# Performance work log

Hardware: AMD Instinct MI355X
Metric: run time of the kernel (lower is better)

## Reference

```python
import jax, jax.numpy as jnp
import numpy as np

B, D, H = 16384, 2048, 16
EPS = 1e-5


def setup_inputs() -> dict:
    key = jax.random.key(0)
    ks = jax.random.split(key, 14)
    s = 0.02
    return {
        "e_a": jax.random.normal(ks[0], (B, D), jnp.float32),
        "e_b": jax.random.normal(ks[1], (B, D), jnp.float32),
        "w_in_ab": jax.random.normal(ks[2], (3 * D, D), jnp.float32) * s,
        "b_in_ab": jnp.zeros((3 * D,), jnp.float32),
        "w_out_ab": jax.random.normal(ks[3], (D, D), jnp.float32) * s,
        "b_out_ab": jnp.zeros((D,), jnp.float32),
        "w_in_ba": jax.random.normal(ks[4], (3 * D, D), jnp.float32) * s,
        "b_in_ba": jnp.zeros((3 * D,), jnp.float32),
        "w_out_ba": jax.random.normal(ks[5], (D, D), jnp.float32) * s,
        "b_out_ba": jnp.zeros((D,), jnp.float32),
        "gamma_a": jnp.ones((D,), jnp.float32),
        "beta_a": jnp.zeros((D,), jnp.float32),
        "gamma_b": jnp.ones((D,), jnp.float32),
        "beta_b": jnp.zeros((D,), jnp.float32),
    }


def _mha_seq1(q_in, kv_in, w_in, b_in, w_out, b_out):
    """torch nn.MultiheadAttention with seq_len=1 for both query and key."""
    b, d = q_in.shape
    hd = d // H
    wq, wk, wv = jnp.split(w_in, 3, axis=0)
    bq, bk, bv = jnp.split(b_in, 3)
    q = (q_in @ wq.T + bq).reshape(b, H, hd)
    k = (kv_in @ wk.T + bk).reshape(b, H, hd)
    v = (kv_in @ wv.T + bv).reshape(b, H, hd)
    scores = jnp.sum(q * k, axis=-1) / jnp.sqrt(jnp.asarray(hd, q.dtype))  # (B,H)
    w = jax.nn.softmax(scores[..., None], axis=-1)  # (B,H,1) == ones (single key)
    attn = (w * v).reshape(b, d)
    out = attn @ w_out.T + b_out
    attn_w = jnp.mean(w, axis=1)[:, None, :]  # (B,1,1), averaged over heads
    return out, attn_w


def _layernorm(x, g, b):
    m = jnp.mean(x, axis=-1, keepdims=True)
    v = jnp.mean((x - m) ** 2, axis=-1, keepdims=True)
    return (x - m) / jnp.sqrt(v + EPS) * g + b


def reference(e_a, e_b, w_in_ab, b_in_ab, w_out_ab, b_out_ab,
              w_in_ba, b_in_ba, w_out_ba, b_out_ba,
              gamma_a, beta_a, gamma_b, beta_b):
    a_attn, attn_w_a = _mha_seq1(e_a, e_b, w_in_ab, b_in_ab, w_out_ab, b_out_ab)
    b_attn, _ = _mha_seq1(e_b, e_a, w_in_ba, b_in_ba, w_out_ba, b_out_ba)
    e_a_prime = _layernorm(e_a + a_attn, gamma_a, beta_a)
    e_b_prime = _layernorm(e_b + b_attn, gamma_b, beta_b)
    return (e_a_prime, e_b_prime, attn_w_a)
```

## Files before the change

### kernel.cpp

```cpp
#include <hip/hip_runtime.h>
#include <hip/hip_bf16.h>
#include <stdint.h>
#include <stddef.h>


static constexpr int B_ROWS = 16384;
static constexpr int DIM    = 2048;
static constexpr float EPS  = 1e-5f;

typedef __bf16 bf16_t;
typedef __bf16 bf16x8 __attribute__((ext_vector_type(8)));
typedef float  f32x4  __attribute__((ext_vector_type(4)));

#define MEMFENCE asm volatile("" ::: "memory")
#define SBAR     __builtin_amdgcn_s_barrier()
#define SCHEDB   __builtin_amdgcn_sched_barrier(0)
#define WAITVM(n) asm volatile("s_waitcnt vmcnt(" #n ")" ::: "memory")

__device__ __forceinline__ void gld_lds16(const bf16_t* g, bf16_t* l) {
  __builtin_amdgcn_global_load_lds(
      (const __attribute__((address_space(1))) void*)g,
      (__attribute__((address_space(3))) void*)l, 16, 0, 0);
}

__global__ __launch_bounds__(256) void k_f32_to_bf16(const float* __restrict__ in,
                                                     bf16_t* __restrict__ out) {
  size_t i = ((size_t)blockIdx.x * 256 + threadIdx.x) * 8;
  f32x4 a = *(const f32x4*)(in + i);
  f32x4 b = *(const f32x4*)(in + i + 4);
  bf16x8 o;
  o[0] = (bf16_t)a[0]; o[1] = (bf16_t)a[1]; o[2] = (bf16_t)a[2]; o[3] = (bf16_t)a[3];
  o[4] = (bf16_t)b[0]; o[5] = (bf16_t)b[1]; o[6] = (bf16_t)b[2]; o[7] = (bf16_t)b[3];
  *(bf16x8*)(out + i) = o;
}

__global__ __launch_bounds__(256) void k_transpose_bf16(const float* __restrict__ W,
                                                        bf16_t* __restrict__ Wt,
                                                        int n) {
  __shared__ float t[32][33];
  const int bx = blockIdx.x * 32, by = blockIdx.y * 32;
  const int tx = threadIdx.x & 31, ty = threadIdx.x >> 5;
  #pragma unroll
  for (int r = ty; r < 32; r += 8)
    t[r][tx] = W[(size_t)(by + r) * n + bx + tx];
  __syncthreads();
  #pragma unroll
  for (int r = ty; r < 32; r += 8)
    Wt[(size_t)(bx + r) * n + by + tx] = (bf16_t)t[tx][r];
}

__global__ __launch_bounds__(256) void k_bias_combine(const float* __restrict__ wout,
                                                      const float* __restrict__ bv,
                                                      const float* __restrict__ bout,
                                                      float* __restrict__ bc, int n) {
  const int i = blockIdx.x;
  const float* row = wout + (size_t)i * n;
  float s = 0.f;
  for (int k = threadIdx.x; k < n; k += 256) s += row[k] * bv[k];
  #pragma unroll
  for (int o = 32; o; o >>= 1) s += __shfl_down(s, o, 64);
  __shared__ float red[4];
  if ((threadIdx.x & 63) == 0) red[threadIdx.x >> 6] = s;
  __syncthreads();
  if (threadIdx.x == 0) bc[i] = red[0] + red[1] + red[2] + red[3] + bout[i];
}

__global__ __launch_bounds__(256) void k_gemm_bt_small(const bf16_t* __restrict__ A,
                                                       const bf16_t* __restrict__ Bt,
                                                       bf16_t* __restrict__ Cb,
                                                       int M, int N, int K) {
  __shared__ bf16_t lA[128 * 32];
  __shared__ bf16_t lB[128 * 32];
  const int tid  = threadIdx.x;
  const int lane = tid & 63;
  const int wid  = tid >> 6;
  const int wm = wid >> 1, wn = wid & 1;
  const int m0 = blockIdx.y * 128, n0 = blockIdx.x * 128;

  const int sr = tid >> 2;
  const int sc = (tid & 3) * 8;
  const bf16_t* gA0 = A  + (size_t)(m0 + sr) * K + sc;
  const bf16_t* gA1 = A  + (size_t)(m0 + 64 + sr) * K + sc;
  const bf16_t* gB0 = Bt + (size_t)(n0 + sr) * K + sc;
  const bf16_t* gB1 = Bt + (size_t)(n0 + 64 + sr) * K + sc;

  f32x4 acc[4][4] = {};
  const int fr = lane & 15;
  const int kh = (lane >> 4) * 8;

  for (int kt = 0; kt < K; kt += 32) {
    gld_lds16(gA0 + kt, lA + tid * 8);
    gld_lds16(gA1 + kt, lA + 2048 + tid * 8);
    gld_lds16(gB0 + kt, lB + tid * 8);
    gld_lds16(gB1 + kt, lB + 2048 + tid * 8);
    __syncthreads();
    bf16x8 af[4], bfv[4];
    #pragma unroll
    for (int i = 0; i < 4; ++i) {
      af[i]  = *(const bf16x8*)(lA + (wm * 64 + i * 16 + fr) * 32 + kh);
      bfv[i] = *(const bf16x8*)(lB + (wn * 64 + i * 16 + fr) * 32 + kh);
    }
    #pragma unroll
    for (int i = 0; i < 4; ++i)
      #pragma unroll
      for (int j = 0; j < 4; ++j)
        acc[i][j] = __builtin_amdgcn_mfma_f32_16x16x32_bf16(af[i], bfv[j], acc[i][j], 0, 0, 0);
    __syncthreads();
  }
  const int cr = (lane >> 4) * 4;
  const int cc = lane & 15;
  #pragma unroll
  for (int i = 0; i < 4; ++i)
    #pragma unroll
    for (int j = 0; j < 4; ++j) {
      const int gm = m0 + wm * 64 + i * 16 + cr;
      const int gn = n0 + wn * 64 + j * 16 + cc;
      #pragma unroll
      for (int r = 0; r < 4; ++r)
        Cb[(size_t)(gm + r) * N + gn] = (bf16_t)acc[i][j][r];
    }
}

__global__ __launch_bounds__(512, 2) void k_gemm256(const bf16_t* __restrict__ A,
                                                    const bf16_t* __restrict__ Bt,
                                                    float* __restrict__ Cf,
                                                    const float* __restrict__ resid,
                                                    const float* __restrict__ bias,
                                                    int M, int N, int K) {
  __shared__ bf16_t lA[2][256 * 64];
  __shared__ bf16_t lB[2][256 * 64];
  const int tid  = threadIdx.x;
  const int lane = tid & 63;
  const int wid  = tid >> 6;
  const int wr = wid >> 2;
  const int wc = wid & 3;

  const int nbx = N >> 8;
  const int nwg = (M >> 8) * nbx;
  const int orig = blockIdx.y * nbx + blockIdx.x;
  const int cpx = nwg >> 3;
  const int swz = (orig & 7) * cpx + (orig >> 3);
  const int m0 = (swz / nbx) << 8;
  const int n0 = (swz % nbx) << 8;

  const int srow  = tid >> 3;
  const int sunit = (tid & 7) ^ ((tid >> 3) & 7);
  const bf16_t* gA = A  + (size_t)(m0 + srow) * K + sunit * 8;
  const bf16_t* gB = Bt + (size_t)(n0 + srow) * K + sunit * 8;
  const size_t cK = (size_t)64 * K;
  const int lofs = tid * 8;

  f32x4 acc[8][4] = {};

  const int NT = K >> 6;

  const int frl = lane & 15;
  const int fxor = lane & 7;
  const int fg  = lane >> 4;

#define LDA(buf, i, kk) \
  (*(const bf16x8*)(&lA[buf][(wr * 128 + (i) * 16 + frl) * 64 + \
                            ((((kk) * 4 + fg) ^ fxor) * 8)]))
#define LDB(buf, j, kk) \
  (*(const bf16x8*)(&lB[buf][(wc * 64 + (j) * 16 + frl) * 64 + \
                            ((((kk) * 4 + fg) ^ fxor) * 8)]))
#define STAGE_A(buf, c, kt) gld_lds16(gA + (size_t)(c) * cK + (kt), \
                                      &lA[buf][(c) * 4096 + lofs])
#define STAGE_B(buf, c, kt) gld_lds16(gB + (size_t)(c) * cK + (kt), \
                                      &lB[buf][(c) * 4096 + lofs])

#define MFMA16(mg, kk)                                                         \
  __builtin_amdgcn_s_setprio(1);                                               \
  _Pragma("unroll")                                                            \
  for (int mi = 0; mi < 4; ++mi) {                                             \
    _Pragma("unroll")                                                          \
    for (int j = 0; j < 4; ++j)                                                \
      acc[(mg) * 4 + mi][j] = __builtin_amdgcn_mfma_f32_16x16x32_bf16(         \
          af[mi], bf[j], acc[(mg) * 4 + mi][j], 0, 0, 0);                      \
  }                                                                            \
  __builtin_amdgcn_s_setprio(0)

  {
    STAGE_B(0, 0, 0); STAGE_B(0, 1, 0); STAGE_B(0, 2, 0); STAGE_B(0, 3, 0);
    STAGE_A(0, 0, 0); STAGE_A(0, 2, 0); STAGE_A(0, 1, 0); STAGE_A(0, 3, 0);
    WAITVM(0); SCHEDB;
    MEMFENCE; SBAR; MEMFENCE;
  }

  bf16x8 bf[4];
  int buf = 0;

  for (int t = 0; t < NT - 1; ++t) {
    const int ktn = (t + 1) << 6;
    const int nb = buf ^ 1;
    {
      bf16x8 af[4];
      #pragma unroll
      for (int mi = 0; mi < 4; ++mi) af[mi] = LDA(buf, mi, 0);
      #pragma unroll
      for (int j = 0; j < 4; ++j) bf[j] = LDB(buf, j, 0);
      STAGE_B(nb, 0, ktn); STAGE_B(nb, 1, ktn);
      MEMFENCE; SBAR; MEMFENCE;
      MFMA16(0, 0);
      WAITVM(2); SCHEDB;
      MEMFENCE; SBAR; MEMFENCE;
    }
    {
      bf16x8 af[4];
      #pragma unroll
      for (int mi = 0; mi < 4; ++mi) af[mi] = LDA(buf, 4 + mi, 0);
      STAGE_B(nb, 2, ktn); STAGE_B(nb, 3, ktn);
      MEMFENCE; SBAR; MEMFENCE;
      MFMA16(1, 0);
      MEMFENCE; SBAR; MEMFENCE;
    }
    {
      bf16x8 af[4];
      #pragma unroll
      for (int mi = 0; mi < 4; ++mi) af[mi] = LDA(buf, mi, 1);
      #pragma unroll
      for (int j = 0; j < 4; ++j) bf[j] = LDB(buf, j, 1);
      STAGE_A(nb, 0, ktn); STAGE_A(nb, 2, ktn);
      MEMFENCE; SBAR; MEMFENCE;
      MFMA16(0, 1);
      MEMFENCE; SBAR; MEMFENCE;
    }
    {
      bf16x8 af[4];
      #pragma unroll
      for (int mi = 0; mi < 4; ++mi) af[mi] = LDA(buf, 4 + mi, 1);
      STAGE_A(nb, 1, ktn); STAGE_A(nb, 3, ktn);
      MEMFENCE; SBAR; MEMFENCE;
      MFMA16(1, 1);
      WAITVM(2); SCHEDB;
      MEMFENCE; SBAR; MEMFENCE;
    }
    buf = nb;
  }

  {
    {
      bf16x8 af[4];
      #pragma unroll
      for (int mi = 0; mi < 4; ++mi) af[mi] = LDA(buf, mi, 0);
      #pragma unroll
      for (int j = 0; j < 4; ++j) bf[j] = LDB(buf, j, 0);
      MEMFENCE; SBAR; MEMFENCE;
      MFMA16(0, 0);
      WAITVM(0); SCHEDB;
      MEMFENCE; SBAR; MEMFENCE;
    }
    {
      bf16x8 af[4];
      #pragma unroll
      for (int mi = 0; mi < 4; ++mi) af[mi] = LDA(buf, 4 + mi, 0);
      MEMFENCE; SBAR; MEMFENCE;
      MFMA16(1, 0);
      MEMFENCE; SBAR; MEMFENCE;
    }
    {
      bf16x8 af[4];
      #pragma unroll
      for (int mi = 0; mi < 4; ++mi) af[mi] = LDA(buf, mi, 1);
      #pragma unroll
      for (int j = 0; j < 4; ++j) bf[j] = LDB(buf, j, 1);
      MEMFENCE; SBAR; MEMFENCE;
      MFMA16(0, 1);
      MEMFENCE; SBAR; MEMFENCE;
    }
    {
      bf16x8 af[4];
      #pragma unroll
      for (int mi = 0; mi < 4; ++mi) af[mi] = LDA(buf, 4 + mi, 1);
      MEMFENCE; SBAR; MEMFENCE;
      MFMA16(1, 1);
    }
  }

  const int cr = (lane >> 4) * 4;
  const int cc = lane & 15;
  #pragma unroll
  for (int i = 0; i < 8; ++i) {
    #pragma unroll
    for (int j = 0; j < 4; ++j) {
      const int gm = m0 + wr * 128 + i * 16 + cr;
      const int gn = n0 + wc * 64 + j * 16 + cc;
      #pragma unroll
      for (int r = 0; r < 4; ++r) {
        const size_t idx = (size_t)(gm + r) * N + gn;
        Cf[idx] = acc[i][j][r] + resid[idx] + bias[gn];
      }
    }
  }
#undef LDA
#undef LDB
#undef STAGE_A
#undef STAGE_B
#undef MFMA16
}

__global__ __launch_bounds__(256) void k_ln(float* __restrict__ io,
                                            const float* __restrict__ gamma_a,
                                            const float* __restrict__ beta_a,
                                            const float* __restrict__ gamma_b,
                                            const float* __restrict__ beta_b) {
  const int row = blockIdx.x;
  const float* gamma = (row < B_ROWS) ? gamma_a : gamma_b;
  const float* beta  = (row < B_ROWS) ? beta_a  : beta_b;
  float* p = io + (size_t)row * DIM;
  const int c0 = threadIdx.x * 8;

  f32x4 x0 = *(f32x4*)(p + c0);
  f32x4 x1 = *(f32x4*)(p + c0 + 4);
  float s = 0.f, sq = 0.f;
  #pragma unroll
  for (int r = 0; r < 4; ++r) {
    s += x0[r] + x1[r];
    sq += x0[r] * x0[r] + x1[r] * x1[r];
  }
  #pragma unroll
  for (int o = 32; o; o >>= 1) {
    s  += __shfl_down(s, o, 64);
    sq += __shfl_down(sq, o, 64);
  }
  __shared__ float rs[4], rq[4];
  if ((threadIdx.x & 63) == 0) { rs[threadIdx.x >> 6] = s; rq[threadIdx.x >> 6] = sq; }
  __syncthreads();
  s  = rs[0] + rs[1] + rs[2] + rs[3];
  sq = rq[0] + rq[1] + rq[2] + rq[3];

  const float mean = s * (1.f / DIM);
  const float var  = sq * (1.f / DIM) - mean * mean;
  const float inv  = rsqrtf(var + EPS);

  f32x4 g0 = *(const f32x4*)(gamma + c0);
  f32x4 g1 = *(const f32x4*)(gamma + c0 + 4);
  f32x4 b0 = *(const f32x4*)(beta + c0);
  f32x4 b1 = *(const f32x4*)(beta + c0 + 4);
  #pragma unroll
  for (int r = 0; r < 4; ++r) {
    x0[r] = (x0[r] - mean) * inv * g0[r] + b0[r];
    x1[r] = (x1[r] - mean) * inv * g1[r] + b1[r];
  }
  *(f32x4*)(p + c0)     = x0;
  *(f32x4*)(p + c0 + 4) = x1;
}

__global__ __launch_bounds__(256) void k_fill_ones(float* __restrict__ p, int n) {
  const int i = blockIdx.x * 256 + threadIdx.x;
  if (i < n) p[i] = 1.0f;
}

extern "C" void kernel_launch(void* const* d_in, const int* in_sizes, int n_in,
                              void* d_out, int out_size, void* d_ws, size_t ws_size,
                              hipStream_t stream) {
  const float* e_a      = (const float*)d_in[0];
  const float* e_b      = (const float*)d_in[1];
  const float* w_in_ab  = (const float*)d_in[2];
  const float* b_in_ab  = (const float*)d_in[3];
  const float* w_out_ab = (const float*)d_in[4];
  const float* b_out_ab = (const float*)d_in[5];
  const float* w_in_ba  = (const float*)d_in[6];
  const float* b_in_ba  = (const float*)d_in[7];
  const float* w_out_ba = (const float*)d_in[8];
  const float* b_out_ba = (const float*)d_in[9];
  const float* gamma_a  = (const float*)d_in[10];
  const float* beta_a   = (const float*)d_in[11];
  const float* gamma_b  = (const float*)d_in[12];
  const float* beta_b   = (const float*)d_in[13];
  float* out = (float*)d_out;

  char* w = (char*)d_ws;
  bf16_t* eA_bf  = (bf16_t*)w; w += (size_t)B_ROWS * DIM * 2;
  bf16_t* eB_bf  = (bf16_t*)w; w += (size_t)B_ROWS * DIM * 2;
  bf16_t* woAB   = (bf16_t*)w; w += (size_t)DIM * DIM * 2;
  bf16_t* woBA   = (bf16_t*)w; w += (size_t)DIM * DIM * 2;
  bf16_t* wvTAB  = (bf16_t*)w; w += (size_t)DIM * DIM * 2;
  bf16_t* wvTBA  = (bf16_t*)w; w += (size_t)DIM * DIM * 2;
  bf16_t* wcAB   = (bf16_t*)w; w += (size_t)DIM * DIM * 2;
  bf16_t* wcBA   = (bf16_t*)w; w += (size_t)DIM * DIM * 2;
  float*  bcAB   = (float*)w;  w += (size_t)DIM * 4;
  float*  bcBA   = (float*)w;  w += (size_t)DIM * 4;

  const size_t nE = (size_t)B_ROWS * DIM;
  const size_t nW = (size_t)DIM * DIM;

  k_f32_to_bf16<<<nE / 2048, 256, 0, stream>>>(e_a, eA_bf);
  k_f32_to_bf16<<<nE / 2048, 256, 0, stream>>>(e_b, eB_bf);
  k_f32_to_bf16<<<nW / 2048, 256, 0, stream>>>(w_out_ab, woAB);
  k_f32_to_bf16<<<nW / 2048, 256, 0, stream>>>(w_out_ba, woBA);
  k_transpose_bf16<<<dim3(64, 64), 256, 0, stream>>>(w_in_ab + 2 * nW, wvTAB, DIM);
  k_transpose_bf16<<<dim3(64, 64), 256, 0, stream>>>(w_in_ba + 2 * nW, wvTBA, DIM);
  k_bias_combine<<<DIM, 256, 0, stream>>>(w_out_ab, b_in_ab + 2 * DIM, b_out_ab, bcAB, DIM);
  k_bias_combine<<<DIM, 256, 0, stream>>>(w_out_ba, b_in_ba + 2 * DIM, b_out_ba, bcBA, DIM);

  k_gemm_bt_small<<<dim3(16, 16), 256, 0, stream>>>(woAB, wvTAB, wcAB, DIM, DIM, DIM);
  k_gemm_bt_small<<<dim3(16, 16), 256, 0, stream>>>(woBA, wvTBA, wcBA, DIM, DIM, DIM);

  k_gemm256<<<dim3(8, 64), 512, 0, stream>>>(eB_bf, wcAB, out,      e_a, bcAB,
                                             B_ROWS, DIM, DIM);
  k_gemm256<<<dim3(8, 64), 512, 0, stream>>>(eA_bf, wcBA, out + nE, e_b, bcBA,
                                             B_ROWS, DIM, DIM);

  k_ln<<<2 * B_ROWS, 256, 0, stream>>>(out, gamma_a, beta_a, gamma_b, beta_b);

  k_fill_ones<<<(B_ROWS + 255) / 256, 256, 0, stream>>>(out + 2 * nE, B_ROWS);
}
```

Measured before the change: 1.071 ms.

## Split-K weight-combine GEMM, merge conversions, reorder staging, grid-stride layernorm

The small weight-combine GEMMs now use an 8-way split-K grid that accumulates with fp32 atomics into a zeroed scratch buffer (aliased over the start of the workspace), followed by a conversion to bf16. The activation and weight f32-to-bf16 conversions are merged into paired launches, and activation conversion happens after the scratch is consumed. The main GEMM's prefetch order is changed to stage A before B, and layernorm becomes a grid-stride loop with fewer blocks. The aim is better occupancy for the small GEMM and fewer launches. The cost is atomic traffic, an extra zero pass and an extra conversion pass.

```diff
diff --git a/kernel.cpp b/kernel.cpp
--- a/kernel.cpp
+++ b/kernel.cpp
@@ -32,6 +32,29 @@
   o[0] = (bf16_t)a[0]; o[1] = (bf16_t)a[1]; o[2] = (bf16_t)a[2]; o[3] = (bf16_t)a[3];
   o[4] = (bf16_t)b[0]; o[5] = (bf16_t)b[1]; o[6] = (bf16_t)b[2]; o[7] = (bf16_t)b[3];
   *(bf16x8*)(out + i) = o;
+}
+
+__global__ __launch_bounds__(256) void k_conv2(const float* __restrict__ inA,
+                                               const float* __restrict__ inB,
+                                               bf16_t* __restrict__ outA,
+                                               bf16_t* __restrict__ outB,
+                                               size_t n) {
+  size_t i = ((size_t)blockIdx.x * 256 + threadIdx.x) * 8;
+  const float* in; bf16_t* out; size_t j;
+  if (i < n) { in = inA; out = outA; j = i; }
+  else       { in = inB; out = outB; j = i - n; }
+  f32x4 a = *(const f32x4*)(in + j);
+  f32x4 b = *(const f32x4*)(in + j + 4);
+  bf16x8 o;
+  o[0] = (bf16_t)a[0]; o[1] = (bf16_t)a[1]; o[2] = (bf16_t)a[2]; o[3] = (bf16_t)a[3];
+  o[4] = (bf16_t)b[0]; o[5] = (bf16_t)b[1]; o[6] = (bf16_t)b[2]; o[7] = (bf16_t)b[3];
+  *(bf16x8*)(out + j) = o;
+}
+
+__global__ __launch_bounds__(256) void k_zero_f32(float* __restrict__ p, size_t n) {
+  const size_t stride = (size_t)gridDim.x * 256 * 4;
+  for (size_t i = ((size_t)blockIdx.x * 256 + threadIdx.x) * 4; i < n; i += stride)
+    *(f32x4*)(p + i) = f32x4{0.f, 0.f, 0.f, 0.f};
 }
 
 __global__ __launch_bounds__(256) void k_transpose_bf16(const float* __restrict__ W,
@@ -65,10 +88,10 @@
   if (threadIdx.x == 0) bc[i] = red[0] + red[1] + red[2] + red[3] + bout[i];
 }
 
-__global__ __launch_bounds__(256) void k_gemm_bt_small(const bf16_t* __restrict__ A,
-                                                       const bf16_t* __restrict__ Bt,
-                                                       bf16_t* __restrict__ Cb,
-                                                       int M, int N, int K) {
+__global__ __launch_bounds__(256) void k_gemm_splitk(const bf16_t* __restrict__ A,
+                                                     const bf16_t* __restrict__ Bt,
+                                                     float* __restrict__ Cf,
+                                                     int M, int N, int K) {
   __shared__ bf16_t lA[128 * 32];
   __shared__ bf16_t lB[128 * 32];
   const int tid  = threadIdx.x;
@@ -76,6 +99,8 @@
   const int wid  = tid >> 6;
   const int wm = wid >> 1, wn = wid & 1;
   const int m0 = blockIdx.y * 128, n0 = blockIdx.x * 128;
+  const int k0 = blockIdx.z * (K >> 3);
+  const int k1 = k0 + (K >> 3);
 
   const int sr = tid >> 2;
   const int sc = (tid & 3) * 8;
@@ -88,7 +113,7 @@
   const int fr = lane & 15;
   const int kh = (lane >> 4) * 8;
 
-  for (int kt = 0; kt < K; kt += 32) {
+  for (int kt = k0; kt < k1; kt += 32) {
     gld_lds16(gA0 + kt, lA + tid * 8);
     gld_lds16(gA1 + kt, lA + 2048 + tid * 8);
     gld_lds16(gB0 + kt, lB + tid * 8);
@@ -117,7 +142,7 @@
       const int gn = n0 + wn * 64 + j * 16 + cc;
       #pragma unroll
       for (int r = 0; r < 4; ++r)
-        Cb[(size_t)(gm + r) * N + gn] = (bf16_t)acc[i][j][r];
+        atomicAdd(&Cf[(size_t)(gm + r) * N + gn], acc[i][j][r]);
     }
 }
 
@@ -181,8 +206,8 @@
   __builtin_amdgcn_s_setprio(0)
 
   {
-    STAGE_B(0, 0, 0); STAGE_B(0, 1, 0); STAGE_B(0, 2, 0); STAGE_B(0, 3, 0);
-    STAGE_A(0, 0, 0); STAGE_A(0, 2, 0); STAGE_A(0, 1, 0); STAGE_A(0, 3, 0);
+    STAGE_A(0, 0, 0); STAGE_A(0, 2, 0); STAGE_B(0, 0, 0); STAGE_B(0, 1, 0);
+    STAGE_B(0, 2, 0); STAGE_B(0, 3, 0); STAGE_A(0, 1, 0); STAGE_A(0, 3, 0);
     WAITVM(0); SCHEDB;
     MEMFENCE; SBAR; MEMFENCE;
   }
@@ -199,7 +224,7 @@
       for (int mi = 0; mi < 4; ++mi) af[mi] = LDA(buf, mi, 0);
       #pragma unroll
       for (int j = 0; j < 4; ++j) bf[j] = LDB(buf, j, 0);
-      STAGE_B(nb, 0, ktn); STAGE_B(nb, 1, ktn);
+      STAGE_A(nb, 0, ktn); STAGE_A(nb, 2, ktn);
       MEMFENCE; SBAR; MEMFENCE;
       MFMA16(0, 0);
       WAITVM(2); SCHEDB;
@@ -209,18 +234,18 @@
       bf16x8 af[4];
       #pragma unroll
       for (int mi = 0; mi < 4; ++mi) af[mi] = LDA(buf, 4 + mi, 0);
+      STAGE_B(nb, 0, ktn); STAGE_B(nb, 1, ktn);
+      MEMFENCE; SBAR; MEMFENCE;
+      MFMA16(1, 0);
+      MEMFENCE; SBAR; MEMFENCE;
+    }
+    {
+      bf16x8 af[4];
+      #pragma unroll
+      for (int mi = 0; mi < 4; ++mi) af[mi] = LDA(buf, mi, 1);
+      #pragma unroll
+      for (int j = 0; j < 4; ++j) bf[j] = LDB(buf, j, 1);
       STAGE_B(nb, 2, ktn); STAGE_B(nb, 3, ktn);
-      MEMFENCE; SBAR; MEMFENCE;
-      MFMA16(1, 0);
-      MEMFENCE; SBAR; MEMFENCE;
-    }
-    {
-      bf16x8 af[4];
-      #pragma unroll
-      for (int mi = 0; mi < 4; ++mi) af[mi] = LDA(buf, mi, 1);
-      #pragma unroll
-      for (int j = 0; j < 4; ++j) bf[j] = LDB(buf, j, 1);
-      STAGE_A(nb, 0, ktn); STAGE_A(nb, 2, ktn);
       MEMFENCE; SBAR; MEMFENCE;
       MFMA16(0, 1);
       MEMFENCE; SBAR; MEMFENCE;
@@ -304,46 +329,48 @@
                                             const float* __restrict__ beta_a,
                                             const float* __restrict__ gamma_b,
                                             const float* __restrict__ beta_b) {
-  const int row = blockIdx.x;
-  const float* gamma = (row < B_ROWS) ? gamma_a : gamma_b;
-  const float* beta  = (row < B_ROWS) ? beta_a  : beta_b;
-  float* p = io + (size_t)row * DIM;
+  __shared__ float rs[4], rq[4];
   const int c0 = threadIdx.x * 8;
-
-  f32x4 x0 = *(f32x4*)(p + c0);
-  f32x4 x1 = *(f32x4*)(p + c0 + 4);
-  float s = 0.f, sq = 0.f;
-  #pragma unroll
-  for (int r = 0; r < 4; ++r) {
-    s += x0[r] + x1[r];
-    sq += x0[r] * x0[r] + x1[r] * x1[r];
-  }
-  #pragma unroll
-  for (int o = 32; o; o >>= 1) {
-    s  += __shfl_down(s, o, 64);
-    sq += __shfl_down(sq, o, 64);
-  }
-  __shared__ float rs[4], rq[4];
-  if ((threadIdx.x & 63) == 0) { rs[threadIdx.x >> 6] = s; rq[threadIdx.x >> 6] = sq; }
-  __syncthreads();
-  s  = rs[0] + rs[1] + rs[2] + rs[3];
-  sq = rq[0] + rq[1] + rq[2] + rq[3];
-
-  const float mean = s * (1.f / DIM);
-  const float var  = sq * (1.f / DIM) - mean * mean;
-  const float inv  = rsqrtf(var + EPS);
-
-  f32x4 g0 = *(const f32x4*)(gamma + c0);
-  f32x4 g1 = *(const f32x4*)(gamma + c0 + 4);
-  f32x4 b0 = *(const f32x4*)(beta + c0);
-  f32x4 b1 = *(const f32x4*)(beta + c0 + 4);
-  #pragma unroll
-  for (int r = 0; r < 4; ++r) {
-    x0[r] = (x0[r] - mean) * inv * g0[r] + b0[r];
-    x1[r] = (x1[r] - mean) * inv * g1[r] + b1[r];
-  }
-  *(f32x4*)(p + c0)     = x0;
-  *(f32x4*)(p + c0 + 4) = x1;
+  for (int row = blockIdx.x; row < 2 * B_ROWS; row += gridDim.x) {
+    const float* gamma = (row < B_ROWS) ? gamma_a : gamma_b;
+    const float* beta  = (row < B_ROWS) ? beta_a  : beta_b;
+    float* p = io + (size_t)row * DIM;
+
+    f32x4 x0 = *(f32x4*)(p + c0);
+    f32x4 x1 = *(f32x4*)(p + c0 + 4);
+    float s = 0.f, sq = 0.f;
+    #pragma unroll
+    for (int r = 0; r < 4; ++r) {
+      s += x0[r] + x1[r];
+      sq += x0[r] * x0[r] + x1[r] * x1[r];
+    }
+    #pragma unroll
+    for (int o = 32; o; o >>= 1) {
+      s  += __shfl_down(s, o, 64);
+      sq += __shfl_down(sq, o, 64);
+    }
+    if ((threadIdx.x & 63) == 0) { rs[threadIdx.x >> 6] = s; rq[threadIdx.x >> 6] = sq; }
+    __syncthreads();
+    s  = rs[0] + rs[1] + rs[2] + rs[3];
+    sq = rq[0] + rq[1] + rq[2] + rq[3];
+
+    const float mean = s * (1.f / DIM);
+    const float var  = sq * (1.f / DIM) - mean * mean;
+    const float inv  = rsqrtf(var + EPS);
+
+    f32x4 g0 = *(const f32x4*)(gamma + c0);
+    f32x4 g1 = *(const f32x4*)(gamma + c0 + 4);
+    f32x4 b0 = *(const f32x4*)(beta + c0);
+    f32x4 b1 = *(const f32x4*)(beta + c0 + 4);
+    #pragma unroll
+    for (int r = 0; r < 4; ++r) {
+      x0[r] = (x0[r] - mean) * inv * g0[r] + b0[r];
+      x1[r] = (x1[r] - mean) * inv * g1[r] + b1[r];
+    }
+    *(f32x4*)(p + c0)     = x0;
+    *(f32x4*)(p + c0 + 4) = x1;
+    __syncthreads();
+  }
 }
 
 __global__ __launch_bounds__(256) void k_fill_ones(float* __restrict__ p, int n) {
@@ -370,39 +397,41 @@
   const float* beta_b   = (const float*)d_in[13];
   float* out = (float*)d_out;
 
-  char* w = (char*)d_ws;
-  bf16_t* eA_bf  = (bf16_t*)w; w += (size_t)B_ROWS * DIM * 2;
-  bf16_t* eB_bf  = (bf16_t*)w; w += (size_t)B_ROWS * DIM * 2;
-  bf16_t* woAB   = (bf16_t*)w; w += (size_t)DIM * DIM * 2;
-  bf16_t* woBA   = (bf16_t*)w; w += (size_t)DIM * DIM * 2;
-  bf16_t* wvTAB  = (bf16_t*)w; w += (size_t)DIM * DIM * 2;
-  bf16_t* wvTBA  = (bf16_t*)w; w += (size_t)DIM * DIM * 2;
-  bf16_t* wcAB   = (bf16_t*)w; w += (size_t)DIM * DIM * 2;
-  bf16_t* wcBA   = (bf16_t*)w; w += (size_t)DIM * DIM * 2;
-  float*  bcAB   = (float*)w;  w += (size_t)DIM * 4;
-  float*  bcBA   = (float*)w;  w += (size_t)DIM * 4;
-
   const size_t nE = (size_t)B_ROWS * DIM;
   const size_t nW = (size_t)DIM * DIM;
 
-  k_f32_to_bf16<<<nE / 2048, 256, 0, stream>>>(e_a, eA_bf);
-  k_f32_to_bf16<<<nE / 2048, 256, 0, stream>>>(e_b, eB_bf);
-  k_f32_to_bf16<<<nW / 2048, 256, 0, stream>>>(w_out_ab, woAB);
-  k_f32_to_bf16<<<nW / 2048, 256, 0, stream>>>(w_out_ba, woBA);
+  char* w = (char*)d_ws;
+  float*  wcf    = (float*)w;
+  bf16_t* eA_bf  = (bf16_t*)w; w += nE * 2;
+  bf16_t* eB_bf  = (bf16_t*)w; w += nE * 2;
+  bf16_t* woAB   = (bf16_t*)w; w += nW * 2;
+  bf16_t* woBA   = (bf16_t*)w; w += nW * 2;
+  bf16_t* wvTAB  = (bf16_t*)w; w += nW * 2;
+  bf16_t* wvTBA  = (bf16_t*)w; w += nW * 2;
+  bf16_t* wcAB   = (bf16_t*)w; w += nW * 2;
+  bf16_t* wcBA   = (bf16_t*)w; w += nW * 2;
+  float*  bcAB   = (float*)w;  w += DIM * 4;
+  float*  bcBA   = (float*)w;  w += DIM * 4;
+
+  k_conv2<<<2 * nW / 2048, 256, 0, stream>>>(w_out_ab, w_out_ba, woAB, woBA, nW);
   k_transpose_bf16<<<dim3(64, 64), 256, 0, stream>>>(w_in_ab + 2 * nW, wvTAB, DIM);
   k_transpose_bf16<<<dim3(64, 64), 256, 0, stream>>>(w_in_ba + 2 * nW, wvTBA, DIM);
   k_bias_combine<<<DIM, 256, 0, stream>>>(w_out_ab, b_in_ab + 2 * DIM, b_out_ab, bcAB, DIM);
   k_bias_combine<<<DIM, 256, 0, stream>>>(w_out_ba, b_in_ba + 2 * DIM, b_out_ba, bcBA, DIM);
-
-  k_gemm_bt_small<<<dim3(16, 16), 256, 0, stream>>>(woAB, wvTAB, wcAB, DIM, DIM, DIM);
-  k_gemm_bt_small<<<dim3(16, 16), 256, 0, stream>>>(woBA, wvTBA, wcBA, DIM, DIM, DIM);
+  k_zero_f32<<<2048, 256, 0, stream>>>(wcf, 2 * nW);
+
+  k_gemm_splitk<<<dim3(16, 16, 8), 256, 0, stream>>>(woAB, wvTAB, wcf,      DIM, DIM, DIM);
+  k_gemm_splitk<<<dim3(16, 16, 8), 256, 0, stream>>>(woBA, wvTBA, wcf + nW, DIM, DIM, DIM);
+  k_f32_to_bf16<<<2 * nW / 2048, 256, 0, stream>>>(wcf, wcAB);
+
+  k_conv2<<<2 * nE / 2048, 256, 0, stream>>>(e_a, e_b, eA_bf, eB_bf, nE);
 
   k_gemm256<<<dim3(8, 64), 512, 0, stream>>>(eB_bf, wcAB, out,      e_a, bcAB,
                                              B_ROWS, DIM, DIM);
   k_gemm256<<<dim3(8, 64), 512, 0, stream>>>(eA_bf, wcBA, out + nE, e_b, bcBA,
                                              B_ROWS, DIM, DIM);
 
-  k_ln<<<2 * B_ROWS, 256, 0, stream>>>(out, gamma_a, beta_a, gamma_b, beta_b);
+  k_ln<<<8192, 256, 0, stream>>>(out, gamma_a, beta_a, gamma_b, beta_b);
 
   k_fill_ones<<<(B_ROWS + 255) / 256, 256, 0, stream>>>(out + 2 * nE, B_ROWS);
 }
```

Result: slower. 1.216 ms (+13.5%).
